# Performance work log

Hardware: AMD Instinct MI355X
Metric: run time of the kernel (lower is better)

## Reference

```python
import jax, jax.numpy as jnp
import numpy as np

N_DST = 100000


def setup_inputs() -> dict:
    key = jax.random.key(0)
    ks = jax.random.split(key, 12)
    R, Ns, E, Din, H = 3, 100000, 1000000, 128, 64
    return {
        "dst_feat": jax.random.normal(ks[0], (N_DST, Din), jnp.float32),
        "neigh_feats": jax.random.normal(ks[1], (R, Ns, Din), jnp.float32),
        "Wt": jax.random.normal(ks[2], (R + 1, Din, H), jnp.float32) * 0.05,
        "bt": jnp.zeros((R + 1, H), jnp.float32),
        "attn_l": jax.random.normal(ks[3], (R, H), jnp.float32) * 0.1,
        "attn_r": jax.random.normal(ks[4], (R, H), jnp.float32) * 0.1,
        "W1": jax.random.normal(ks[5], (H, 128), jnp.float32) * 0.1,
        "b1": jnp.zeros((128,), jnp.float32),
        "w2": jax.random.normal(ks[6], (128, 1), jnp.float32) * 0.1,
        "src_idx": jax.random.randint(ks[7], (R, E), 0, Ns, jnp.int32),
        "dst_idx": jax.random.randint(ks[8], (R, E), 0, N_DST, jnp.int32),
    }


def _gat_relation(h_src, h_dst, al, ar, src, dst):
    # el/er: per-node attention logits (dot with attn vectors)
    el = h_src @ al  # [Ns]
    er = h_dst @ ar  # [Nd]
    e = jax.nn.leaky_relu(el[src] + er[dst], 0.01)  # [E]
    # edge softmax per destination node (segment softmax)
    m = jax.ops.segment_max(e, dst, num_segments=N_DST)
    a = jnp.exp(e - m[dst])
    s = jax.ops.segment_sum(a, dst, num_segments=N_DST)
    a = a / s[dst]
    # weighted aggregation: sum_e a_e * h_src[src_e]
    out = jax.ops.segment_sum(h_src[src] * a[:, None], dst, num_segments=N_DST)
    return jax.nn.elu(out)


def reference(dst_feat, neigh_feats, Wt, bt, attn_l, attn_r, W1, b1, w2, src_idx, dst_idx):
    R = neigh_feats.shape[0]
    h_dst = dst_feat @ Wt[0] + bt[0]  # weight_T[0]
    z_r = []
    for r in range(R):
        h_src = neigh_feats[r] @ Wt[r + 1] + bt[r + 1]
        z_r.append(_gat_relation(h_src, h_dst, attn_l[r], attn_r[r], src_idx[r], dst_idx[r]))
    z_r = jnp.stack(z_r, axis=1)  # [N, R, D]
    # semantic attention
    w = (jnp.tanh(z_r @ W1 + b1) @ w2).mean(axis=0)  # [R, 1]
    a_w = jax.nn.softmax(w, axis=0)  # softmax over relations
    z = (z_r * a_w[None]).sum(axis=1)  # [N, D]
    return z
```

## Files before the change

### kernel.cpp

```cpp
#include <hip/hip_runtime.h>
#include <hip/hip_fp16.h>

#define N_DST 100000
#define DIN 128
#define HDIM 64
#define RREL 3
#define NE 1000000

#define NBKT_REL 196
#define NBKT (RREL * NBKT_REL)
#define NSEG (RREL * N_DST)
#define EDGE_CHUNK 16384
#define NBLK_BIN ((RREL * NE + EDGE_CHUNK - 1) / EDGE_CHUNK)

typedef _Float16 f16x8 __attribute__((ext_vector_type(8)));
typedef float f32x4 __attribute__((ext_vector_type(4)));

__global__ __launch_bounds__(256) void k_gemm(
    const float* __restrict__ dst_feat, const float* __restrict__ neigh,
    const float* __restrict__ Wt, const float* __restrict__ bt,
    const float* __restrict__ attn_l, const float* __restrict__ attn_r,
    __half* __restrict__ h16, float* __restrict__ el, float* __restrict__ er) {
  const int RB = (N_DST + 127) / 128;
  int mat = blockIdx.x / RB;
  int row0 = (blockIdx.x % RB) * 128;
  const float* A = (mat == 0) ? dst_feat : (neigh + (size_t)(mat - 1) * N_DST * DIN);
  const float* W = Wt + (size_t)mat * DIN * HDIM;
  const float* b = bt + mat * HDIM;

  __shared__ __align__(16) unsigned char lds[48 * 1024];
  unsigned char* ldsA = lds;
  unsigned char* ldsW = lds + 32768;

  int tid = threadIdx.x;

#pragma unroll
  for (int i = 0; i < 8; i++) {
    int s = tid + 256 * i;
    int row = s >> 4;
    int kb = s & 15;
    int gr = row0 + row;
    if (gr >= N_DST) gr = N_DST - 1;
    const float* ap = A + (size_t)gr * DIN + kb * 8;
    float4 v0 = *(const float4*)ap;
    float4 v1 = *(const float4*)(ap + 4);
    f16x8 hv;
    hv[0] = (_Float16)v0.x; hv[1] = (_Float16)v0.y;
    hv[2] = (_Float16)v0.z; hv[3] = (_Float16)v0.w;
    hv[4] = (_Float16)v1.x; hv[5] = (_Float16)v1.y;
    hv[6] = (_Float16)v1.z; hv[7] = (_Float16)v1.w;
    *(f16x8*)(ldsA + row * 256 + ((kb * 16) ^ ((row & 7) << 4))) = hv;
  }

  {
    int col = tid & 63;
    int kq = tid >> 6;
    const float* wp = W + (size_t)(kq * 32) * HDIM + col;
    float wr[32];
#pragma unroll
    for (int m = 0; m < 32; m++) wr[m] = wp[(size_t)m * HDIM];
#pragma unroll
    for (int m8 = 0; m8 < 4; m8++) {
      f16x8 hv;
#pragma unroll
      for (int j = 0; j < 8; j++) hv[j] = (_Float16)wr[m8 * 8 + j];
      int byt = kq * 64 + m8 * 16;
      *(f16x8*)(ldsW + col * 256 + (byt ^ ((col & 7) << 4))) = hv;
    }
  }
  __syncthreads();

  int w = tid >> 6;
  int l = tid & 63;
  int li = l & 15;
  int hi = l >> 4;
  f32x4 acc[2][4] = {};
#pragma unroll
  for (int ks = 0; ks < 4; ks++) {
    int kbyte = ks * 64 + hi * 16;
    f16x8 af[2], bf[4];
#pragma unroll
    for (int rt = 0; rt < 2; rt++) {
      int row = w * 32 + rt * 16 + li;
      af[rt] = *(f16x8*)(ldsA + row * 256 + (kbyte ^ ((row & 7) << 4)));
    }
#pragma unroll
    for (int ct = 0; ct < 4; ct++) {
      int col = ct * 16 + li;
      bf[ct] = *(f16x8*)(ldsW + col * 256 + (kbyte ^ ((col & 7) << 4)));
    }
#pragma unroll
    for (int rt = 0; rt < 2; rt++)
#pragma unroll
      for (int ct = 0; ct < 4; ct++)
        acc[rt][ct] = __builtin_amdgcn_mfma_f32_16x16x32_f16(af[rt], bf[ct], acc[rt][ct], 0, 0, 0);
  }

  float bv[4];
#pragma unroll
  for (int ct = 0; ct < 4; ct++) bv[ct] = b[ct * 16 + li];
#pragma unroll
  for (int rt = 0; rt < 2; rt++)
#pragma unroll
    for (int ct = 0; ct < 4; ct++)
#pragma unroll
      for (int j = 0; j < 4; j++) acc[rt][ct][j] += bv[ct];

  if (mat == 0) {
#pragma unroll
    for (int r = 0; r < RREL; r++) {
      float av[4];
#pragma unroll
      for (int ct = 0; ct < 4; ct++) av[ct] = attn_r[r * HDIM + ct * 16 + li];
#pragma unroll
      for (int rt = 0; rt < 2; rt++) {
        float p[4];
#pragma unroll
        for (int j = 0; j < 4; j++)
          p[j] = acc[rt][0][j] * av[0] + acc[rt][1][j] * av[1] +
                 acc[rt][2][j] * av[2] + acc[rt][3][j] * av[3];
#pragma unroll
        for (int o = 1; o < 16; o <<= 1)
#pragma unroll
          for (int j = 0; j < 4; j++) p[j] += __shfl_xor(p[j], o);
        if (li == 0) {
#pragma unroll
          for (int j = 0; j < 4; j++) {
            int gr = row0 + w * 32 + rt * 16 + hi * 4 + j;
            if (gr < N_DST) er[r * N_DST + gr] = p[j];
          }
        }
      }
    }
  } else {
    int r = mat - 1;
    float av[4];
#pragma unroll
    for (int ct = 0; ct < 4; ct++) av[ct] = attn_l[r * HDIM + ct * 16 + li];
#pragma unroll
    for (int rt = 0; rt < 2; rt++) {
      float p[4];
#pragma unroll
      for (int j = 0; j < 4; j++)
        p[j] = acc[rt][0][j] * av[0] + acc[rt][1][j] * av[1] +
               acc[rt][2][j] * av[2] + acc[rt][3][j] * av[3];
#pragma unroll
      for (int o = 1; o < 16; o <<= 1)
#pragma unroll
        for (int j = 0; j < 4; j++) p[j] += __shfl_xor(p[j], o);
      if (li == 0) {
#pragma unroll
        for (int j = 0; j < 4; j++) {
          int gr = row0 + w * 32 + rt * 16 + hi * 4 + j;
          if (gr < N_DST) el[r * N_DST + gr] = p[j];
        }
      }
    }
    __half* hb = h16 + (size_t)r * N_DST * HDIM;
#pragma unroll
    for (int rt = 0; rt < 2; rt++)
#pragma unroll
      for (int j = 0; j < 4; j++) {
        int gr = row0 + w * 32 + rt * 16 + hi * 4 + j;
        if (gr < N_DST) {
#pragma unroll
          for (int ct = 0; ct < 4; ct++)
            hb[(size_t)gr * HDIM + ct * 16 + li] = __float2half(acc[rt][ct][j]);
        }
      }
  }
}


__global__ __launch_bounds__(256) void k_hist(const int* __restrict__ dst_idx,
                                              int* __restrict__ hist) {
  __shared__ int h[NBKT];
  int tid = threadIdx.x;
  int blk = blockIdx.x;
  for (int i = tid; i < NBKT; i += 256) h[i] = 0;
  __syncthreads();
  int e0 = blk * EDGE_CHUNK;
  int e1 = min(e0 + EDGE_CHUNK, RREL * NE);
  for (int idx = e0 + tid; idx < e1; idx += 256) {
    int r = idx / NE;
    int d = dst_idx[idx];
    atomicAdd(&h[r * NBKT_REL + (d >> 9)], 1);
  }
  __syncthreads();
  for (int i = tid; i < NBKT; i += 256)
    hist[(size_t)i * NBLK_BIN + blk] = h[i];
}

__global__ __launch_bounds__(256) void k_colscan(int* __restrict__ hist,
                                                 int* __restrict__ bcounts) {
  __shared__ int sm[256];
  int b = blockIdx.x;
  int tid = threadIdx.x;
  int v = (tid < NBLK_BIN) ? hist[(size_t)b * NBLK_BIN + tid] : 0;
  sm[tid] = v;
  __syncthreads();
  for (int off = 1; off < 256; off <<= 1) {
    int t = (tid >= off) ? sm[tid - off] : 0;
    __syncthreads();
    sm[tid] += t;
    __syncthreads();
  }
  if (tid < NBLK_BIN) hist[(size_t)b * NBLK_BIN + tid] = sm[tid] - v;
  if (tid == 255) bcounts[b] = sm[255];
}

__global__ __launch_bounds__(256) void k_bscan(const int* __restrict__ bcounts,
                                               int* __restrict__ bucket_base,
                                               int* __restrict__ offsets) {
  __shared__ int sm[256];
  int tid = threadIdx.x;
  int base = tid * 3;
  int c[3];
#pragma unroll
  for (int k = 0; k < 3; k++) c[k] = (base + k < NBKT) ? bcounts[base + k] : 0;
  int tsum = c[0] + c[1] + c[2];
  sm[tid] = tsum;
  __syncthreads();
  for (int off = 1; off < 256; off <<= 1) {
    int v = (tid >= off) ? sm[tid - off] : 0;
    __syncthreads();
    sm[tid] += v;
    __syncthreads();
  }
  int run = sm[tid] - tsum;
#pragma unroll
  for (int k = 0; k < 3; k++) {
    if (base + k < NBKT) bucket_base[base + k] = run;
    run += c[k];
  }
  if (tid == 255) bucket_base[NBKT] = sm[255];
  if (tid == 0) offsets[NSEG] = RREL * NE;
}

__global__ __launch_bounds__(256) void k_place(const int* __restrict__ src_idx,
                                               const int* __restrict__ dst_idx,
                                               const int* __restrict__ hist,
                                               const int* __restrict__ bucket_base,
                                               unsigned* __restrict__ tmp) {
  __shared__ int cur[NBKT];
  int tid = threadIdx.x;
  int blk = blockIdx.x;
  for (int i = tid; i < NBKT; i += 256)
    cur[i] = bucket_base[i] + hist[(size_t)i * NBLK_BIN + blk];
  __syncthreads();
  int e0 = blk * EDGE_CHUNK;
  int e1 = min(e0 + EDGE_CHUNK, RREL * NE);
  for (int idx = e0 + tid; idx < e1; idx += 256) {
    int r = idx / NE;
    int d = dst_idx[idx];
    int s = src_idx[idx];
    int bucket = r * NBKT_REL + (d >> 9);
    int pos = atomicAdd(&cur[bucket], 1);
    tmp[pos] = ((unsigned)(d & 511) << 17) | (unsigned)s;
  }
}

__global__ __launch_bounds__(256) void k_bucket_csr(
    const int* __restrict__ bucket_base, const unsigned* __restrict__ tmp,
    int* __restrict__ src_sorted, int* __restrict__ offsets) {
  __shared__ int cnt[512];
  __shared__ int base_l[512];
  __shared__ int sm[256];
  int b = blockIdx.x;
  int r = b / NBKT_REL;
  int brel = b - r * NBKT_REL;
  int gbase = bucket_base[b];
  int gend = bucket_base[b + 1];
  int tid = threadIdx.x;
  cnt[tid] = 0;
  cnt[tid + 256] = 0;
  __syncthreads();
  for (int e = gbase + tid; e < gend; e += 256)
    atomicAdd(&cnt[tmp[e] >> 17], 1);
  __syncthreads();
  int c0 = cnt[2 * tid], c1 = cnt[2 * tid + 1];
  int tsum = c0 + c1;
  sm[tid] = tsum;
  __syncthreads();
  for (int off = 1; off < 256; off <<= 1) {
    int v = (tid >= off) ? sm[tid - off] : 0;
    __syncthreads();
    sm[tid] += v;
    __syncthreads();
  }
  int run = sm[tid] - tsum;
  base_l[2 * tid] = run;
  base_l[2 * tid + 1] = run + c0;
  __syncthreads();
  for (int s = tid; s < 512; s += 256) {
    int dst = (brel << 9) + s;
    if (dst < N_DST) offsets[r * N_DST + dst] = gbase + base_l[s];
    cnt[s] = 0;
  }
  __syncthreads();
  for (int e = gbase + tid; e < gend; e += 256) {
    unsigned w = tmp[e];
    int s = w >> 17;
    int pos = gbase + base_l[s] + atomicAdd(&cnt[s], 1);
    src_sorted[pos] = (int)(w & 0x1FFFFu);
  }
}

__global__ __launch_bounds__(256) void k_aggregate(
    const int* __restrict__ offsets, const int* __restrict__ src_sorted,
    const float* __restrict__ el, const float* __restrict__ er,
    const __half* __restrict__ h16, float* __restrict__ zbuf) {
  int gw = blockIdx.x * 32 + (threadIdx.x >> 3);
  int li = threadIdx.x & 7;
  if (gw >= NSEG) return;
  int r = gw / N_DST;
  int start = offsets[gw], end = offsets[gw + 1];
  float erv = er[gw];
  const unsigned char* hs = (const unsigned char*)(h16 + (size_t)r * N_DST * HDIM);
  const float* elr = el + (size_t)r * N_DST;
  float acc[8] = {};
  float ssum = 0.f;
  int sNext = (start < end) ? src_sorted[start] : 0;
  for (int e = start; e < end; ++e) {
    int s = sNext;
    if (e + 1 < end) sNext = src_sorted[e + 1];
    float x = elr[s] + erv;
    float4 rv = *(const float4*)(hs + (unsigned)(s * 128 + li * 16));
    x = (x > 0.f) ? x : 0.01f * x;
    float a = __expf(x);
    ssum += a;
    const __half2* hp = (const __half2*)&rv;
#pragma unroll
    for (int q = 0; q < 4; q++) {
      float2 f = __half22float2(hp[q]);
      acc[2 * q] += a * f.x;
      acc[2 * q + 1] += a * f.y;
    }
  }
  float inv = (end > start) ? 1.f / ssum : 0.f;
  float zv[8];
#pragma unroll
  for (int q = 0; q < 8; q++) {
    float v = acc[q] * inv;
    zv[q] = (v > 0.f) ? v : (__expf(v) - 1.f);
  }
  float* zp = zbuf + (size_t)gw * HDIM + li * 8;
  *(float4*)zp = make_float4(zv[0], zv[1], zv[2], zv[3]);
  *(float4*)(zp + 4) = make_float4(zv[4], zv[5], zv[6], zv[7]);
}

__global__ __launch_bounds__(256) void k_semantic(
    const float* __restrict__ zbuf, const float* __restrict__ W1,
    const float* __restrict__ b1, const float* __restrict__ w2,
    float* __restrict__ w_acc) {
  __shared__ __align__(16) unsigned char lds[32 * 1024];
  unsigned char* ldsZ = lds;
  unsigned char* ldsW = lds + 16384;
  __shared__ float wsum[RREL];
  int tid = threadIdx.x;
  if (tid < RREL) wsum[tid] = 0.f;
  int row0 = blockIdx.x * 128;

  {
    int col = tid & 127;
    int kq = tid >> 7;
    const float* wp = W1 + (size_t)(kq * 32) * 128 + col;
    float wr[32];
#pragma unroll
    for (int m = 0; m < 32; m++) wr[m] = wp[(size_t)m * 128];
#pragma unroll
    for (int m8 = 0; m8 < 4; m8++) {
      f16x8 hv;
#pragma unroll
      for (int j = 0; j < 8; j++) hv[j] = (_Float16)wr[m8 * 8 + j];
      int byt = kq * 64 + m8 * 16;
      *(f16x8*)(ldsW + col * 128 + (byt ^ ((col & 7) << 4))) = hv;
    }
  }
#pragma unroll
  for (int i = 0; i < 4; i++) {
    int s = tid + 256 * i;
    int row = s >> 3;
    int kb = s & 7;
    int gr = row0 + row;
    if (gr >= NSEG) gr = NSEG - 1;
    const float* zp = zbuf + (size_t)gr * HDIM + kb * 8;
    float4 v0 = *(const float4*)zp;
    float4 v1 = *(const float4*)(zp + 4);
    f16x8 hv;
    hv[0] = (_Float16)v0.x; hv[1] = (_Float16)v0.y;
    hv[2] = (_Float16)v0.z; hv[3] = (_Float16)v0.w;
    hv[4] = (_Float16)v1.x; hv[5] = (_Float16)v1.y;
    hv[6] = (_Float16)v1.z; hv[7] = (_Float16)v1.w;
    *(f16x8*)(ldsZ + row * 128 + ((kb * 16) ^ ((row & 7) << 4))) = hv;
  }
  __syncthreads();

  int w = tid >> 6;
  int l = tid & 63;
  int li = l & 15;
  int hi = l >> 4;
  f32x4 acc[2][8] = {};
#pragma unroll
  for (int ks = 0; ks < 2; ks++) {
    int kbyte = ks * 64 + hi * 16;
    f16x8 af[2], bf[8];
#pragma unroll
    for (int rt = 0; rt < 2; rt++) {
      int row = w * 32 + rt * 16 + li;
      af[rt] = *(f16x8*)(ldsZ + row * 128 + (kbyte ^ ((row & 7) << 4)));
    }
#pragma unroll
    for (int ct = 0; ct < 8; ct++) {
      int col = ct * 16 + li;
      bf[ct] = *(f16x8*)(ldsW + col * 128 + (kbyte ^ ((col & 7) << 4)));
    }
#pragma unroll
    for (int rt = 0; rt < 2; rt++)
#pragma unroll
      for (int ct = 0; ct < 8; ct++)
        acc[rt][ct] = __builtin_amdgcn_mfma_f32_16x16x32_f16(af[rt], bf[ct], acc[rt][ct], 0, 0, 0);
  }

  float p[2][4] = {};
#pragma unroll
  for (int ct = 0; ct < 8; ct++) {
    float b1v = b1[ct * 16 + li];
    float w2v = w2[ct * 16 + li];
#pragma unroll
    for (int rt = 0; rt < 2; rt++)
#pragma unroll
      for (int j = 0; j < 4; j++) {
        float x = acc[rt][ct][j] + b1v;
        float ex = __expf(2.f * x);
        p[rt][j] += (1.f - 2.f / (ex + 1.f)) * w2v;
      }
  }
#pragma unroll
  for (int o = 1; o < 16; o <<= 1)
#pragma unroll
    for (int rt = 0; rt < 2; rt++)
#pragma unroll
      for (int j = 0; j < 4; j++) p[rt][j] += __shfl_xor(p[rt][j], o);
  if (li == 0) {
#pragma unroll
    for (int rt = 0; rt < 2; rt++)
#pragma unroll
      for (int j = 0; j < 4; j++) {
        int row = row0 + w * 32 + rt * 16 + hi * 4 + j;
        if (row < NSEG) atomicAdd(&wsum[row / N_DST], p[rt][j]);
      }
  }
  __syncthreads();
  if (tid < RREL) atomicAdd(&w_acc[tid], wsum[tid]);
}

__global__ __launch_bounds__(256) void k_final(const float* __restrict__ zbuf,
                                               const float* __restrict__ w_acc,
                                               float* __restrict__ out) {
  int idx = blockIdx.x * 256 + threadIdx.x;
  if (idx >= N_DST * HDIM / 4) return;
  const float invN = 1.0f / N_DST;
  float w0 = w_acc[0] * invN, w1 = w_acc[1] * invN, w2v = w_acc[2] * invN;
  float m = fmaxf(w0, fmaxf(w1, w2v));
  float e0 = __expf(w0 - m), e1 = __expf(w1 - m), e2 = __expf(w2v - m);
  float inv = 1.f / (e0 + e1 + e2);
  e0 *= inv; e1 *= inv; e2 *= inv;
  size_t o = (size_t)idx * 4;
  const size_t stride = (size_t)N_DST * HDIM;
  float4 z0 = *(const float4*)(zbuf + o);
  float4 z1 = *(const float4*)(zbuf + stride + o);
  float4 z2 = *(const float4*)(zbuf + 2 * stride + o);
  float4 r;
  r.x = e0 * z0.x + e1 * z1.x + e2 * z2.x;
  r.y = e0 * z0.y + e1 * z1.y + e2 * z2.y;
  r.z = e0 * z0.z + e1 * z1.z + e2 * z2.z;
  r.w = e0 * z0.w + e1 * z1.w + e2 * z2.w;
  *(float4*)(out + o) = r;
}

extern "C" void kernel_launch(void* const* d_in, const int* in_sizes, int n_in,
                              void* d_out, int out_size, void* d_ws, size_t ws_size,
                              hipStream_t stream) {
  const float* dst_feat = (const float*)d_in[0];
  const float* neigh = (const float*)d_in[1];
  const float* Wt = (const float*)d_in[2];
  const float* bt = (const float*)d_in[3];
  const float* attn_l = (const float*)d_in[4];
  const float* attn_r = (const float*)d_in[5];
  const float* W1 = (const float*)d_in[6];
  const float* b1 = (const float*)d_in[7];
  const float* w2 = (const float*)d_in[8];
  const int* src_idx = (const int*)d_in[9];
  const int* dst_idx = (const int*)d_in[10];
  float* out = (float*)d_out;

  char* p = (char*)d_ws;
  auto alloc = [&](size_t bytes) {
    char* q = p;
    p += (bytes + 255) & ~(size_t)255;
    return (void*)q;
  };
  __half* h16 = (__half*)alloc((size_t)RREL * N_DST * HDIM * 2);
  float* el = (float*)alloc((size_t)RREL * N_DST * 4);
  float* er = (float*)alloc((size_t)RREL * N_DST * 4);
  float* zbuf = (float*)alloc((size_t)RREL * N_DST * HDIM * 4);
  float* w_acc = (float*)alloc(64);
  int* offsets = (int*)alloc(((size_t)NSEG + 1) * 4);
  int* hist = (int*)alloc((size_t)NBKT * NBLK_BIN * 4);
  int* bcounts = (int*)alloc((size_t)NBKT * 4);
  int* bucket_base = (int*)alloc((size_t)(NBKT + 1) * 4);
  unsigned* tmp = (unsigned*)alloc((size_t)RREL * NE * 4);
  int* src_sorted = (int*)alloc((size_t)RREL * NE * 4);

  hipMemsetAsync(w_acc, 0, 64, stream);

  k_gemm<<<4 * ((N_DST + 127) / 128), 256, 0, stream>>>(dst_feat, neigh, Wt, bt, attn_l, attn_r,
                                                        h16, el, er);
  k_hist<<<NBLK_BIN, 256, 0, stream>>>(dst_idx, hist);
  k_colscan<<<NBKT, 256, 0, stream>>>(hist, bcounts);
  k_bscan<<<1, 256, 0, stream>>>(bcounts, bucket_base, offsets);
  k_place<<<NBLK_BIN, 256, 0, stream>>>(src_idx, dst_idx, hist, bucket_base, tmp);
  k_bucket_csr<<<NBKT, 256, 0, stream>>>(bucket_base, tmp, src_sorted, offsets);
  k_aggregate<<<(NSEG + 31) / 32, 256, 0, stream>>>(offsets, src_sorted, el, er, h16, zbuf);
  k_semantic<<<(NSEG + 127) / 128, 256, 0, stream>>>(zbuf, W1, b1, w2, w_acc);
  k_final<<<(N_DST * HDIM / 4 + 255) / 256, 256, 0, stream>>>(zbuf, w_acc, out);
}
```

Measured before the change: 506.1 us.

## Precompute fp16 swizzled weights and load A fragments directly into registers

A small prep kernel converts the weight matrices to fp16 once, already in the swizzled LDS layout, so each GEMM block only copies 16KB instead of doing strided fp32 loads and conversion. The A tile is no longer staged through LDS; each lane loads its MFMA fragment rows straight from global memory into registers, with software prefetch of the next K slice overlapped with the MFMAs. This shrinks LDS use from 48KB to 16KB, which may raise occupancy. The trade-offs are one extra kernel launch and less coalesced global reads of A, since each lane reads 32-byte pieces from scattered rows.

New measurement: 511.8 us. About the same (+1.1%).

```diff
diff --git a/kernel.cpp b/kernel.cpp
--- a/kernel.cpp
+++ b/kernel.cpp
@@ -16,85 +16,92 @@
 typedef _Float16 f16x8 __attribute__((ext_vector_type(8)));
 typedef float f32x4 __attribute__((ext_vector_type(4)));
 
+__global__ __launch_bounds__(256) void k_wprep(const float* __restrict__ Wt,
+                                               __half* __restrict__ W16) {
+  int g = blockIdx.x * 256 + threadIdx.x;
+  int col = g & 63;
+  int kb = (g >> 6) & 15;
+  int mat = g >> 10;
+  const float* wp = Wt + ((size_t)mat * DIN + kb * 8) * HDIM + col;
+  f16x8 hv;
+#pragma unroll
+  for (int j = 0; j < 8; j++) hv[j] = (_Float16)wp[(size_t)j * HDIM];
+  *(f16x8*)((unsigned char*)W16 + mat * 16384 + col * 256 + ((kb * 16) ^ ((col & 7) << 4))) = hv;
+}
+
 __global__ __launch_bounds__(256) void k_gemm(
     const float* __restrict__ dst_feat, const float* __restrict__ neigh,
-    const float* __restrict__ Wt, const float* __restrict__ bt,
+    const __half* __restrict__ W16, const float* __restrict__ bt,
     const float* __restrict__ attn_l, const float* __restrict__ attn_r,
     __half* __restrict__ h16, float* __restrict__ el, float* __restrict__ er) {
   const int RB = (N_DST + 127) / 128;
   int mat = blockIdx.x / RB;
   int row0 = (blockIdx.x % RB) * 128;
   const float* A = (mat == 0) ? dst_feat : (neigh + (size_t)(mat - 1) * N_DST * DIN);
-  const float* W = Wt + (size_t)mat * DIN * HDIM;
   const float* b = bt + mat * HDIM;
 
-  __shared__ __align__(16) unsigned char lds[48 * 1024];
-  unsigned char* ldsA = lds;
-  unsigned char* ldsW = lds + 32768;
-
-  int tid = threadIdx.x;
-
-#pragma unroll
-  for (int i = 0; i < 8; i++) {
-    int s = tid + 256 * i;
-    int row = s >> 4;
-    int kb = s & 15;
-    int gr = row0 + row;
-    if (gr >= N_DST) gr = N_DST - 1;
-    const float* ap = A + (size_t)gr * DIN + kb * 8;
-    float4 v0 = *(const float4*)ap;
-    float4 v1 = *(const float4*)(ap + 4);
-    f16x8 hv;
-    hv[0] = (_Float16)v0.x; hv[1] = (_Float16)v0.y;
-    hv[2] = (_Float16)v0.z; hv[3] = (_Float16)v0.w;
-    hv[4] = (_Float16)v1.x; hv[5] = (_Float16)v1.y;
-    hv[6] = (_Float16)v1.z; hv[7] = (_Float16)v1.w;
-    *(f16x8*)(ldsA + row * 256 + ((kb * 16) ^ ((row & 7) << 4))) = hv;
-  }
+  __shared__ __align__(16) unsigned char ldsW[16384];
+  int tid = threadIdx.x;
 
   {
-    int col = tid & 63;
-    int kq = tid >> 6;
-    const float* wp = W + (size_t)(kq * 32) * HDIM + col;
-    float wr[32];
-#pragma unroll
-    for (int m = 0; m < 32; m++) wr[m] = wp[(size_t)m * HDIM];
-#pragma unroll
-    for (int m8 = 0; m8 < 4; m8++) {
-      f16x8 hv;
-#pragma unroll
-      for (int j = 0; j < 8; j++) hv[j] = (_Float16)wr[m8 * 8 + j];
-      int byt = kq * 64 + m8 * 16;
-      *(f16x8*)(ldsW + col * 256 + (byt ^ ((col & 7) << 4))) = hv;
-    }
-  }
-  __syncthreads();
+    const float4* wsrc = (const float4*)((const unsigned char*)W16 + (size_t)mat * 16384);
+#pragma unroll
+    for (int i = 0; i < 4; i++)
+      *(float4*)(ldsW + (tid + 256 * i) * 16) = wsrc[tid + 256 * i];
+  }
 
   int w = tid >> 6;
   int l = tid & 63;
   int li = l & 15;
   int hi = l >> 4;
+
+  int r0 = row0 + w * 32 + li;
+  int ra = min(r0, N_DST - 1);
+  int rb = min(r0 + 16, N_DST - 1);
+  const float* pa = A + (size_t)ra * DIN + hi * 8;
+  const float* pb = A + (size_t)rb * DIN + hi * 8;
+
+  auto cvt8 = [](const float4& v0, const float4& v1) {
+    f16x8 h;
+    h[0] = (_Float16)v0.x; h[1] = (_Float16)v0.y;
+    h[2] = (_Float16)v0.z; h[3] = (_Float16)v0.w;
+    h[4] = (_Float16)v1.x; h[5] = (_Float16)v1.y;
+    h[6] = (_Float16)v1.z; h[7] = (_Float16)v1.w;
+    return h;
+  };
+
+  float4 sa0[2], sb0[2], sa1[2], sb1[2];
+  sa0[0] = *(const float4*)(pa);      sa0[1] = *(const float4*)(pa + 4);
+  sb0[0] = *(const float4*)(pb);      sb0[1] = *(const float4*)(pb + 4);
+  sa1[0] = *(const float4*)(pa + 32); sa1[1] = *(const float4*)(pa + 36);
+  sb1[0] = *(const float4*)(pb + 32); sb1[1] = *(const float4*)(pb + 36);
+
+  __syncthreads();
+
   f32x4 acc[2][4] = {};
-#pragma unroll
-  for (int ks = 0; ks < 4; ks++) {
-    int kbyte = ks * 64 + hi * 16;
-    f16x8 af[2], bf[4];
-#pragma unroll
-    for (int rt = 0; rt < 2; rt++) {
-      int row = w * 32 + rt * 16 + li;
-      af[rt] = *(f16x8*)(ldsA + row * 256 + (kbyte ^ ((row & 7) << 4)));
-    }
-#pragma unroll
-    for (int ct = 0; ct < 4; ct++) {
-      int col = ct * 16 + li;
-      bf[ct] = *(f16x8*)(ldsW + col * 256 + (kbyte ^ ((col & 7) << 4)));
-    }
-#pragma unroll
-    for (int rt = 0; rt < 2; rt++)
-#pragma unroll
-      for (int ct = 0; ct < 4; ct++)
-        acc[rt][ct] = __builtin_amdgcn_mfma_f32_16x16x32_f16(af[rt], bf[ct], acc[rt][ct], 0, 0, 0);
-  }
+#define KS_STEP(KS, SA, SB, PREF_OFF, DO_PREF)                                  \
+  {                                                                             \
+    f16x8 afa = cvt8(SA[0], SA[1]);                                             \
+    f16x8 afb = cvt8(SB[0], SB[1]);                                             \
+    if (DO_PREF) {                                                              \
+      SA[0] = *(const float4*)(pa + PREF_OFF);                                  \
+      SA[1] = *(const float4*)(pa + PREF_OFF + 4);                              \
+      SB[0] = *(const float4*)(pb + PREF_OFF);                                  \
+      SB[1] = *(const float4*)(pb + PREF_OFF + 4);                              \
+    }                                                                           \
+    int kbyte = (KS)*64 + hi * 16;                                              \
+    _Pragma("unroll") for (int ct = 0; ct < 4; ct++) {                          \
+      int col = ct * 16 + li;                                                   \
+      f16x8 bf = *(f16x8*)(ldsW + col * 256 + (kbyte ^ ((col & 7) << 4)));      \
+      acc[0][ct] = __builtin_amdgcn_mfma_f32_16x16x32_f16(afa, bf, acc[0][ct], 0, 0, 0); \
+      acc[1][ct] = __builtin_amdgcn_mfma_f32_16x16x32_f16(afb, bf, acc[1][ct], 0, 0, 0); \
+    }                                                                           \
+  }
+  KS_STEP(0, sa0, sb0, 64, 1)
+  KS_STEP(1, sa1, sb1, 96, 1)
+  KS_STEP(2, sa0, sb0, 0, 0)
+  KS_STEP(3, sa1, sb1, 0, 0)
+#undef KS_STEP
 
   float bv[4];
 #pragma unroll
@@ -502,6 +509,7 @@
     return (void*)q;
   };
   __half* h16 = (__half*)alloc((size_t)RREL * N_DST * HDIM * 2);
+  __half* W16 = (__half*)alloc((size_t)(RREL + 1) * HDIM * DIN * 2);
   float* el = (float*)alloc((size_t)RREL * N_DST * 4);
   float* er = (float*)alloc((size_t)RREL * N_DST * 4);
   float* zbuf = (float*)alloc((size_t)RREL * N_DST * HDIM * 4);
@@ -515,7 +523,8 @@
 
   hipMemsetAsync(w_acc, 0, 64, stream);
 
-  k_gemm<<<4 * ((N_DST + 127) / 128), 256, 0, stream>>>(dst_feat, neigh, Wt, bt, attn_l, attn_r,
+  k_wprep<<<16, 256, 0, stream>>>(Wt, W16);
+  k_gemm<<<4 * ((N_DST + 127) / 128), 256, 0, stream>>>(dst_feat, neigh, W16, bt, attn_l, attn_r,
                                                         h16, el, er);
   k_hist<<<NBLK_BIN, 256, 0, stream>>>(dst_idx, hist);
   k_colscan<<<NBKT, 256, 0, stream>>>(hist, bcounts);
```
